# Kernel tuning notes

Measured on AMD Instinct MI355X. Metric: run time of the kernel, lower is better.

Reference implementation:

```python
import jax, jax.numpy as jnp
import numpy as np

IN_DIM = 128
OUT_DIM = 256
N_ETYPES = 4
N_STEPS = 8
B = 128
N_NODES = 256
E = 393216
CONCAT = IN_DIM + OUT_DIM


def _conv1d(x, w, b):
    # x: [B, C, L], w: [O, I, K] -> valid conv, stride 1
    y = jax.lax.conv_general_dilated(x, w, (1,), 'VALID', dimension_numbers=('NCH', 'OIH', 'NCH'))
    return y + b[None, :, None]


def _maxpool1d(x, k, s):
    return jax.lax.reduce_window(x, -jnp.inf, jax.lax.max, (1, 1, k), (1, 1, s), 'VALID')


def setup_inputs():
    key = jax.random.key(0)
    ks = jax.random.split(key, 16)
    Nn = B * N_NODES
    sc = 0.05
    f32 = jnp.float32
    return {
        'features': jax.random.normal(ks[0], (Nn, IN_DIM), f32),
        'src': jax.random.randint(ks[1], (E,), 0, Nn),
        'dst': jax.random.randint(ks[2], (E,), 0, Nn),
        'etype': jax.random.randint(ks[3], (E,), 0, N_ETYPES),
        'W_msg': jax.random.normal(ks[4], (N_ETYPES, OUT_DIM, OUT_DIM), f32) * sc,
        'b_msg': jnp.zeros((N_ETYPES, OUT_DIM), f32),
        'gru_Wi': jax.random.normal(ks[5], (OUT_DIM, 3 * OUT_DIM), f32) * sc,
        'gru_Wh': jax.random.normal(ks[6], (OUT_DIM, 3 * OUT_DIM), f32) * sc,
        'gru_bi': jnp.zeros((3 * OUT_DIM,), f32),
        'gru_bh': jnp.zeros((3 * OUT_DIM,), f32),
        'conv1_w': jax.random.normal(ks[7], (OUT_DIM, OUT_DIM, 3), f32) * sc,
        'conv1_b': jnp.zeros((OUT_DIM,), f32),
        'conv2_w': jax.random.normal(ks[8], (OUT_DIM, OUT_DIM, 1), f32) * sc,
        'conv2_b': jnp.zeros((OUT_DIM,), f32),
        'convc1_w': jax.random.normal(ks[9], (CONCAT, CONCAT, 3), f32) * sc,
        'convc1_b': jnp.zeros((CONCAT,), f32),
        'convc2_w': jax.random.normal(ks[10], (CONCAT, CONCAT, 1), f32) * sc,
        'convc2_b': jnp.zeros((CONCAT,), f32),
        'wy': jax.random.normal(ks[11], (OUT_DIM, 1), f32) * sc,
        'by': jnp.zeros((1,), f32),
        'wz': jax.random.normal(ks[12], (CONCAT, 1), f32) * sc,
        'bz': jnp.zeros((1,), f32),
        'num_graphs': B,
    }


def reference(features, src, dst, etype, W_msg, b_msg, gru_Wi, gru_Wh, gru_bi, gru_bh,
              conv1_w, conv1_b, conv2_w, conv2_b, convc1_w, convc1_b, convc2_w, convc2_b,
              wy, by, wz, bz, num_graphs):
    Nn = features.shape[0]
    # DGL GatedGraphConv: pad input feats up to out_feats
    h = jnp.pad(features, ((0, 0), (0, OUT_DIM - IN_DIM)))
    for _ in range(N_STEPS):
        # per-etype linear transform of all nodes: [Nn, T, O]
        H_all = jnp.einsum('nd,tdo->nto', h, W_msg) + b_msg[None]
        msg = H_all[src, etype]                              # [E, O]
        a = jax.ops.segment_sum(msg, dst, num_segments=Nn)   # [Nn, O]
        gi = a @ gru_Wi + gru_bi
        gh = h @ gru_Wh + gru_bh
        ir, iz, ig = jnp.split(gi, 3, axis=-1)
        hr, hz, hg = jnp.split(gh, 3, axis=-1)
        r = jax.nn.sigmoid(ir + hr)
        z = jax.nn.sigmoid(iz + hz)
        g = jnp.tanh(ig + r * hg)
        h = (1.0 - z) * g + z * h
    x_i = features.reshape(num_graphs, -1, IN_DIM)
    h_i = h.reshape(num_graphs, -1, OUT_DIM)
    c_i = jnp.concatenate([h_i, x_i], axis=-1)
    Y1 = _maxpool1d(jax.nn.relu(_conv1d(h_i.transpose(0, 2, 1), conv1_w, conv1_b)), 3, 2)
    Y2 = _maxpool1d(jax.nn.relu(_conv1d(Y1, conv2_w, conv2_b)), 2, 2).transpose(0, 2, 1)
    Z1 = _maxpool1d(jax.nn.relu(_conv1d(c_i.transpose(0, 2, 1), convc1_w, convc1_b)), 3, 2)
    Z2 = _maxpool1d(jax.nn.relu(_conv1d(Z1, convc2_w, convc2_b)), 2, 2).transpose(0, 2, 1)
    before_avg = (Y2 @ wy + by) * (Z2 @ wz + bz)   # [B, L, 1]
    avg = before_avg.mean(axis=1)                    # [B, 1]
    return jax.nn.sigmoid(avg).squeeze(-1)           # [B]
```

## Files before the change

kernel.cpp:

```cpp
#include <hip/hip_runtime.h>

#define DEV static __device__ __forceinline__

typedef float f32x4 __attribute__((ext_vector_type(4)));
typedef __bf16 bf16x8 __attribute__((ext_vector_type(8)));
typedef unsigned int u32x4 __attribute__((ext_vector_type(4)));
typedef unsigned int u32x2 __attribute__((ext_vector_type(2)));

#define NNODE 32768
#define NEDGE 393216

DEV unsigned short f2bf(float f) {
    unsigned int u = __builtin_bit_cast(unsigned int, f);
    u += 0x7FFFu + ((u >> 16) & 1u);
    return (unsigned short)(u >> 16);
}
DEV float bf2f(unsigned int b) {
    unsigned int u = b << 16;
    return __builtin_bit_cast(float, u);
}
DEV unsigned int pk2(float a, float b) {
    return (unsigned int)f2bf(a) | ((unsigned int)f2bf(b) << 16);
}
DEV float sigf(float x) { return 1.f / (1.f + __expf(-x)); }

DEV void gld16(const void* g, void* l) {
    __builtin_amdgcn_global_load_lds(
        (const __attribute__((address_space(1))) void*)(g),
        (__attribute__((address_space(3))) void*)(l),
        16, 0, 0);
}


__global__ __launch_bounds__(256) void init_k(
    const float* __restrict__ feat,
    unsigned short* __restrict__ hb0, unsigned short* __restrict__ hb1,
    unsigned short* __restrict__ fb)
{
    int idx = blockIdx.x * 256 + threadIdx.x;
    int r = idx >> 8, c = idx & 255;
    float f = 0.f;
    if (r < NNODE && c < 128) f = feat[(size_t)r * 128 + c];
    unsigned short v = f2bf(f);
    hb0[(size_t)r * 256 + c] = v;
    hb1[(size_t)r * 256 + c] = v;
    if (c < 128) fb[(size_t)r * 128 + c] = v;
}

__global__ __launch_bounds__(256) void prep_wmsg_k(
    const float* __restrict__ Wm, unsigned short* __restrict__ WT)
{
    int idx = blockIdx.x * 256 + threadIdx.x;
    int j = idx >> 8, d = idx & 255;
    int t = j >> 8, o = j & 255;
    WT[idx] = f2bf(Wm[t * 65536 + d * 256 + o]);
}

__global__ __launch_bounds__(256) void prep_gru_k(
    const float* __restrict__ Wi, const float* __restrict__ Wh,
    unsigned short* __restrict__ B2T)
{
    int idx = blockIdx.x * 256 + threadIdx.x;
    int j = idx >> 9, k = idx & 511;
    int band = j >> 6, g = (j >> 4) & 3, ch = (band << 4) + (j & 15);
    float v = 0.f;
    if (g == 0) v = (k < 256) ? Wi[k * 768 + ch] : Wh[(k - 256) * 768 + ch];
    else if (g == 1) v = (k < 256) ? Wi[k * 768 + 256 + ch] : Wh[(k - 256) * 768 + 256 + ch];
    else if (g == 2) { if (k < 256) v = Wi[k * 768 + 512 + ch]; }
    else { if (k >= 256) v = Wh[(k - 256) * 768 + 512 + ch]; }
    B2T[idx] = f2bf(v);
}

__global__ __launch_bounds__(256) void prep_bias2_k(
    const float* __restrict__ bi, const float* __restrict__ bh,
    float* __restrict__ b2)
{
    int j = blockIdx.x * 256 + threadIdx.x;
    int band = j >> 6, g = (j >> 4) & 3, ch = (band << 4) + (j & 15);
    float v;
    if (g == 0) v = bi[ch] + bh[ch];
    else if (g == 1) v = bi[256 + ch] + bh[256 + ch];
    else if (g == 2) v = bi[512 + ch];
    else v = bh[512 + ch];
    b2[j] = v;
}

__global__ __launch_bounds__(256) void prep_conv_k(
    const float* __restrict__ c1w, const float* __restrict__ c2w,
    const float* __restrict__ cc1w, const float* __restrict__ cc2w,
    unsigned short* __restrict__ BTY, unsigned short* __restrict__ BT2,
    unsigned short* __restrict__ BTZ, unsigned short* __restrict__ BTc2)
{
    int idx = blockIdx.x * 256 + threadIdx.x;
    if (idx < 196608) {
        int o = idx / 768, kk = idx - o * 768, k = kk >> 8, c = kk & 255;
        BTY[idx] = f2bf(c1w[o * 768 + c * 3 + k]);
    } else if (idx < 262144) {
        int r = idx - 196608, o = r >> 8, c = r & 255;
        BT2[r] = f2bf(c2w[o * 256 + c]);
    } else if (idx < 704512) {
        int jx = idx - 262144, o = jx / 1152, kk = jx - o * 1152;
        float v;
        if (kk < 768) { int k = kk >> 8, c = kk & 255; v = cc1w[o * 1152 + c * 3 + k]; }
        else { int r = kk - 768, kf = r >> 7, cf = r & 127; v = cc1w[o * 1152 + (256 + cf) * 3 + kf]; }
        BTZ[jx] = f2bf(v);
    } else {
        int r = idx - 704512, o = r / 384, c = r - o * 384;
        BTc2[r] = f2bf(cc2w[o * 384 + c]);
    }
}


__global__ __launch_bounds__(256) void count_k(
    const int* __restrict__ dst, int* __restrict__ cnt)
{
    int e = blockIdx.x * 256 + threadIdx.x;
    atomicAdd(&cnt[dst[e]], 1);
}

__global__ __launch_bounds__(1024) void scan1_k(
    const int* __restrict__ cnt, int* __restrict__ rp, int* __restrict__ bsum)
{
    __shared__ int buf[1024];
    int b = blockIdx.x, tid = threadIdx.x;
    int n = (b << 10) + tid;
    int v = cnt[n];
    buf[tid] = v;
    __syncthreads();
    for (int off = 1; off < 1024; off <<= 1) {
        int x = (tid >= off) ? buf[tid - off] : 0;
        __syncthreads();
        buf[tid] += x;
        __syncthreads();
    }
    rp[n] = buf[tid] - v;
    if (tid == 1023) bsum[b] = buf[1023];
}

__global__ __launch_bounds__(64) void scan2_k(
    const int* __restrict__ bsum, int* __restrict__ boff, int* __restrict__ rp)
{
    int lane = threadIdx.x;
    int v = (lane < 32) ? bsum[lane] : 0;
    int s = v;
    #pragma unroll
    for (int off = 1; off < 32; off <<= 1) {
        int x = __shfl_up(s, off, 64);
        if (lane >= off) s += x;
    }
    if (lane < 32) boff[lane] = s - v;
    if (lane == 31) rp[NNODE] = s;
}

__global__ __launch_bounds__(1024) void scan3_k(
    int* __restrict__ rp, const int* __restrict__ boff)
{
    int b = blockIdx.x, tid = threadIdx.x;
    rp[(b << 10) + tid] += boff[b];
}

__global__ __launch_bounds__(256) void fill_k(
    const int* __restrict__ src, const int* __restrict__ dst,
    const int* __restrict__ et, const int* __restrict__ rp,
    int* __restrict__ pos, int* __restrict__ edat)
{
    int e = blockIdx.x * 256 + threadIdx.x;
    int d = dst[e];
    int p = atomicAdd(&pos[d], 1);
    edat[rp[d] + p] = src[e] | (et[e] << 20);
}


__global__ __launch_bounds__(256) void agg2_k(
    const int* __restrict__ rp, const int* __restrict__ edat,
    const unsigned short* __restrict__ Hmsg, unsigned short* __restrict__ Aonly)
{
    int wave = threadIdx.x >> 6, lane = threadIdx.x & 63;
    int n = (blockIdx.x << 2) + wave;
    int e0 = rp[n], e1 = rp[n + 1];
    float a0 = 0.f, a1 = 0.f, a2 = 0.f, a3 = 0.f;
    const unsigned short* hc = Hmsg + (lane << 2);
    int e = e0;
    for (; e + 8 <= e1; e += 8) {
        u32x2 v[8];
        #pragma unroll
        for (int q = 0; q < 8; q++) {
            int d = edat[e + q];
            v[q] = *(const u32x2*)(hc + ((size_t)(d & 0xFFFFF) << 10) + ((d >> 20) << 8));
        }
        #pragma unroll
        for (int q = 0; q < 8; q++) {
            a0 += bf2f(v[q].x & 0xFFFFu); a1 += bf2f(v[q].x >> 16);
            a2 += bf2f(v[q].y & 0xFFFFu); a3 += bf2f(v[q].y >> 16);
        }
    }
    for (; e < e1; e++) {
        int d = edat[e];
        u32x2 v = *(const u32x2*)(hc + ((size_t)(d & 0xFFFFF) << 10) + ((d >> 20) << 8));
        a0 += bf2f(v.x & 0xFFFFu); a1 += bf2f(v.x >> 16);
        a2 += bf2f(v.y & 0xFFFFu); a3 += bf2f(v.y >> 16);
    }
    u32x2 p; p.x = pk2(a0, a1); p.y = pk2(a2, a3);
    *(u32x2*)(Aonly + (size_t)n * 256 + (lane << 2)) = p;
}

#define STAGE_COORDS                                            \
    int srow[4], scb[4], soff[4];                               \
    _Pragma("unroll")                                           \
    for (int p = 0; p < 4; p++) {                               \
        int c = wave + p * 4;                                   \
        int half = c >> 3, cc = c & 7;                          \
        srow[p] = cc * 16 + (lane >> 2);                        \
        scb[p] = (((lane & 3) ^ ((lane >> 3) & 3)) + half * 4) * 8; \
        soff[p] = half * 4096 + cc * 512;                       \
    }

#define MFMA64(AS, BS)                                                        \
    _Pragma("unroll")                                                         \
    for (int h = 0; h < 2; h++) {                                             \
        bf16x8 af[4], bfr[4];                                                 \
        _Pragma("unroll")                                                     \
        for (int i = 0; i < 4; i++)                                           \
            af[i] = *(const bf16x8*)(&AS[h * 4096 + (qm + i * 16 + fm) * 32 + fksw * 8]); \
        _Pragma("unroll")                                                     \
        for (int i = 0; i < 4; i++)                                           \
            bfr[i] = *(const bf16x8*)(&BS[h * 4096 + (qn + i * 16 + fm) * 32 + fksw * 8]); \
        _Pragma("unroll")                                                     \
        for (int i = 0; i < 4; i++)                                           \
            _Pragma("unroll")                                                 \
            for (int j = 0; j < 4; j++)                                       \
                acc[i][j] = __builtin_amdgcn_mfma_f32_16x16x32_bf16(bfr[j], af[i], acc[i][j], 0, 0, 0); \
    }

__global__ __launch_bounds__(256) void gemm_bt(
    const unsigned short* __restrict__ A, int lda,
    const unsigned short* __restrict__ Bt,
    unsigned short* __restrict__ Cb, int ldcb,
    const float* __restrict__ bias,
    int N, int K, int swz, int relu)
{
    __shared__ __align__(16) unsigned short As[128 * 64];
    __shared__ __align__(16) unsigned short Bs[128 * 64];
    const int tid = threadIdx.x;
    int id = blockIdx.x;
    if (swz) { int per = gridDim.x >> 3; id = (id & 7) * per + (id >> 3); }
    const int nb = N >> 7;
    const int bm = id / nb, bn = id - bm * nb;
    const int wave = tid >> 6, lane = tid & 63;
    const unsigned short* Ag = A + (size_t)(bm * 128) * lda;
    const unsigned short* Bg = Bt + (size_t)(bn * 128) * K;
    const int qm = (wave & 1) << 6, qn = (wave >> 1) << 6;
    const int fm = lane & 15, fkv = lane >> 4;
    const int fksw = fkv ^ ((fm >> 1) & 3);
    STAGE_COORDS

    f32x4 acc[4][4] = {};

    for (int kb = 0; kb < K; kb += 64) {
        __syncthreads();
        #pragma unroll
        for (int p = 0; p < 4; p++)
            gld16(Ag + (size_t)srow[p] * lda + kb + scb[p], As + soff[p]);
        #pragma unroll
        for (int p = 0; p < 4; p++)
            gld16(Bg + (size_t)srow[p] * K + kb + scb[p], Bs + soff[p]);
        __syncthreads();
        MFMA64(As, Bs)
    }

    const int m0 = bm * 128 + qm + fm;
    const int n0 = bn * 128 + qn + (fkv << 2);
    #pragma unroll
    for (int i = 0; i < 4; i++) {
        int row = m0 + i * 16;
        #pragma unroll
        for (int j = 0; j < 4; j++) {
            int col = n0 + j * 16;
            float v0 = acc[i][j][0], v1 = acc[i][j][1],
                  v2 = acc[i][j][2], v3 = acc[i][j][3];
            if (bias) {
                float4 bv = *(const float4*)(bias + col);
                v0 += bv.x; v1 += bv.y; v2 += bv.z; v3 += bv.w;
            }
            if (relu) {
                v0 = fmaxf(v0, 0.f); v1 = fmaxf(v1, 0.f);
                v2 = fmaxf(v2, 0.f); v3 = fmaxf(v3, 0.f);
            }
            u32x2 p; p.x = pk2(v0, v1); p.y = pk2(v2, v3);
            *(u32x2*)(Cb + (size_t)row * ldcb + col) = p;
        }
    }
}

__global__ __launch_bounds__(256) void gemm_conv(
    const unsigned short* __restrict__ Ah,
    const unsigned short* __restrict__ Af,
    const unsigned short* __restrict__ Bt,
    unsigned short* __restrict__ Cb, int ldcb,
    const float* __restrict__ bias,
    int N, int K)
{
    __shared__ __align__(16) unsigned short As[128 * 64];
    __shared__ __align__(16) unsigned short Bs[128 * 64];
    const int tid = threadIdx.x;
    int id = blockIdx.x;
    { int per = gridDim.x >> 3; id = (id & 7) * per + (id >> 3); }
    const int nb = N >> 7;
    const int bm = id / nb, bn = id - bm * nb;
    const int wave = tid >> 6, lane = tid & 63;
    const unsigned short* Bg = Bt + (size_t)(bn * 128) * K;
    const int qm = (wave & 1) << 6, qn = (wave >> 1) << 6;
    const int fm = lane & 15, fkv = lane >> 4;
    const int fksw = fkv ^ ((fm >> 1) & 3);
    STAGE_COORDS

    f32x4 acc[4][4] = {};

    for (int kb = 0; kb < K; kb += 64) {
        const unsigned short* base; int ldA, col, shift;
        if (kb < 768) { base = Ah; ldA = 256; shift = kb >> 8; col = kb & 255; }
        else { int r = kb - 768; base = Af; ldA = 128; shift = r >> 7; col = r & 127; }
        const unsigned short* Ag = base + (size_t)(bm * 128 + shift) * ldA + col;
        __syncthreads();
        #pragma unroll
        for (int p = 0; p < 4; p++)
            gld16(Ag + (size_t)srow[p] * ldA + scb[p], As + soff[p]);
        #pragma unroll
        for (int p = 0; p < 4; p++)
            gld16(Bg + (size_t)srow[p] * K + kb + scb[p], Bs + soff[p]);
        __syncthreads();
        MFMA64(As, Bs)
    }

    const int m0 = bm * 128 + qm + fm;
    const int n0 = bn * 128 + qn + (fkv << 2);
    #pragma unroll
    for (int i = 0; i < 4; i++) {
        int row = m0 + i * 16;
        #pragma unroll
        for (int j = 0; j < 4; j++) {
            int col = n0 + j * 16;
            float4 bv = *(const float4*)(bias + col);
            float v0 = fmaxf(acc[i][j][0] + bv.x, 0.f);
            float v1 = fmaxf(acc[i][j][1] + bv.y, 0.f);
            float v2 = fmaxf(acc[i][j][2] + bv.z, 0.f);
            float v3 = fmaxf(acc[i][j][3] + bv.w, 0.f);
            u32x2 p; p.x = pk2(v0, v1); p.y = pk2(v2, v3);
            *(u32x2*)(Cb + (size_t)row * ldcb + col) = p;
        }
    }
}

__global__ __launch_bounds__(256) void gemm_gru(
    const unsigned short* __restrict__ Aonly,
    const unsigned short* __restrict__ hbc,
    const unsigned short* __restrict__ Bt,
    const float* __restrict__ b2p,
    unsigned short* __restrict__ hbn)
{
    __shared__ __align__(16) unsigned short As[128 * 64];
    __shared__ __align__(16) unsigned short Bs[128 * 64];
    const int tid = threadIdx.x;
    int id = blockIdx.x;
    { int per = gridDim.x >> 3; id = (id & 7) * per + (id >> 3); }
    const int bm = id >> 3;
    const int bn = id & 7;
    const int wave = tid >> 6, lane = tid & 63;
    const unsigned short* Bg = Bt + (size_t)(bn * 128) * 512;
    const int qm = (wave & 1) << 6, qn = (wave >> 1) << 6;
    const int fm = lane & 15, fkv = lane >> 4;
    const int fksw = fkv ^ ((fm >> 1) & 3);
    STAGE_COORDS

    f32x4 acc[4][4] = {};

    #pragma unroll
    for (int kb = 0; kb < 512; kb += 64) {
        const unsigned short* base = (kb < 256) ? Aonly : hbc;
        const unsigned short* Ag = base + (size_t)(bm * 128) * 256 + (kb & 255);
        __syncthreads();
        #pragma unroll
        for (int p = 0; p < 4; p++)
            gld16(Ag + (size_t)srow[p] * 256 + scb[p], As + soff[p]);
        #pragma unroll
        for (int p = 0; p < 4; p++)
            gld16(Bg + (size_t)srow[p] * 512 + kb + scb[p], Bs + soff[p]);
        __syncthreads();
        MFMA64(As, Bs)
    }

    const int band = (bn << 1) + (qn >> 6);
    const int chb = (band << 4) + (fkv << 2);
    const float4 brv = *(const float4*)(b2p + (band << 6) + 0  + (fkv << 2));
    const float4 bzv = *(const float4*)(b2p + (band << 6) + 16 + (fkv << 2));
    const float4 bgv = *(const float4*)(b2p + (band << 6) + 32 + (fkv << 2));
    const float4 bhv = *(const float4*)(b2p + (band << 6) + 48 + (fkv << 2));
    const float br_[4] = {brv.x, brv.y, brv.z, brv.w};
    const float bz_[4] = {bzv.x, bzv.y, bzv.z, bzv.w};
    const float bg_[4] = {bgv.x, bgv.y, bgv.z, bgv.w};
    const float bh_[4] = {bhv.x, bhv.y, bhv.z, bhv.w};
    const int m0 = bm * 128 + qm + fm;
    #pragma unroll
    for (int i = 0; i < 4; i++) {
        int row = m0 + i * 16;
        u32x2 hv = *(const u32x2*)(hbc + (size_t)row * 256 + chb);
        float hp[4] = {bf2f(hv.x & 0xFFFFu), bf2f(hv.x >> 16),
                       bf2f(hv.y & 0xFFFFu), bf2f(hv.y >> 16)};
        float hn[4];
        #pragma unroll
        for (int r = 0; r < 4; r++) {
            float rg = sigf(acc[i][0][r] + br_[r]);
            float zz = sigf(acc[i][1][r] + bz_[r]);
            float pre = acc[i][2][r] + bg_[r] + rg * (acc[i][3][r] + bh_[r]);
            pre = fminf(fmaxf(pre, -15.f), 15.f);
            float t = __expf(2.f * pre);
            float gq = (t - 1.f) / (t + 1.f);
            hn[r] = (1.f - zz) * gq + zz * hp[r];
        }
        u32x2 p; p.x = pk2(hn[0], hn[1]); p.y = pk2(hn[2], hn[3]);
        *(u32x2*)(hbn + (size_t)row * 256 + chb) = p;
    }
}

__global__ __launch_bounds__(256) void pool_k(
    const unsigned short* __restrict__ in, int ldin, int Lb_in, int L_out,
    int win, int C,
    unsigned short* __restrict__ ob, int ldo)
{
    int idx = blockIdx.x * 256 + threadIdx.x;
    int c = idx % C;
    int row = idx / C;
    int b = row / L_out, lp = row - b * L_out;
    const unsigned short* p = in + (size_t)(b * Lb_in + 2 * lp) * ldin + c;
    float m = bf2f(p[0]);
    for (int d = 1; d < win; d++) m = fmaxf(m, bf2f(p[(size_t)d * ldin]));
    ob[(size_t)row * ldo + c] = f2bf(m);
}

__global__ __launch_bounds__(64) void final_k(
    const unsigned short* __restrict__ CY, const unsigned short* __restrict__ CZ,
    const float* __restrict__ wy, const float* __restrict__ by,
    const float* __restrict__ wz, const float* __restrict__ bz,
    float* __restrict__ out)
{
    int b = blockIdx.x, lane = threadIdx.x;
    float val = 0.f;
    if (lane < 63) {
        const unsigned short* y0 = CY + (size_t)(b * 126 + 2 * lane) * 256;
        const unsigned short* y1 = y0 + 256;
        float y = 0.f;
        for (int o = 0; o < 256; o++)
            y += fmaxf(bf2f(y0[o]), bf2f(y1[o])) * wy[o];
        y += by[0];
        const unsigned short* z0 = CZ + (size_t)(b * 126 + 2 * lane) * 384;
        const unsigned short* z1 = z0 + 384;
        float z = 0.f;
        for (int o = 0; o < 384; o++)
            z += fmaxf(bf2f(z0[o]), bf2f(z1[o])) * wz[o];
        z += bz[0];
        val = y * z;
    }
    for (int off = 32; off > 0; off >>= 1) val += __shfl_down(val, off, 64);
    if (lane == 0) out[b] = sigf(val * (1.f / 63.f));
}


extern "C" void kernel_launch(void* const* d_in, const int* in_sizes, int n_in,
                              void* d_out, int out_size, void* d_ws, size_t ws_size,
                              hipStream_t stream)
{
    const float* feat = (const float*)d_in[0];
    const int* src = (const int*)d_in[1];
    const int* dst = (const int*)d_in[2];
    const int* et  = (const int*)d_in[3];
    const float* Wm  = (const float*)d_in[4];
    const float* bm  = (const float*)d_in[5];
    const float* Wi  = (const float*)d_in[6];
    const float* Wh  = (const float*)d_in[7];
    const float* bi  = (const float*)d_in[8];
    const float* bh  = (const float*)d_in[9];
    const float* c1w = (const float*)d_in[10];
    const float* c1b = (const float*)d_in[11];
    const float* c2w = (const float*)d_in[12];
    const float* c2b = (const float*)d_in[13];
    const float* cc1w = (const float*)d_in[14];
    const float* cc1b = (const float*)d_in[15];
    const float* cc2w = (const float*)d_in[16];
    const float* cc2b = (const float*)d_in[17];
    const float* wy = (const float*)d_in[18];
    const float* by = (const float*)d_in[19];
    const float* wz = (const float*)d_in[20];
    const float* bz = (const float*)d_in[21];
    float* out = (float*)d_out;

    char* w = (char*)d_ws;
    size_t off = 0;
    auto alloc = [&](size_t bytes) -> char* {
        char* p = w + off; off += (bytes + 255) & ~(size_t)255; return p;
    };
    unsigned short* hb0 = (unsigned short*)alloc((size_t)(NNODE + 8) * 256 * 2);
    unsigned short* hb1 = (unsigned short*)alloc((size_t)(NNODE + 8) * 256 * 2);
    unsigned short* fb  = (unsigned short*)alloc((size_t)(NNODE + 8) * 128 * 2);
    unsigned short* Aonly = (unsigned short*)alloc((size_t)NNODE * 256 * 2);
    char* R = alloc((size_t)NNODE * 1024 * 2);
    unsigned short* Hmsg = (unsigned short*)R;
    unsigned short* CbY  = (unsigned short*)R;
    unsigned short* CbZ  = (unsigned short*)(R + (size_t)NNODE * 256 * 2);
    unsigned short* P    = (unsigned short*)alloc((size_t)16128 * 384 * 2);
    unsigned short* Cb2Y = (unsigned short*)alloc((size_t)16128 * 256 * 2);
    unsigned short* Cb2Z = (unsigned short*)alloc((size_t)16128 * 384 * 2);
    unsigned short* WT   = (unsigned short*)alloc(1024 * 256 * 2);
    unsigned short* B2T  = (unsigned short*)alloc(1024 * 512 * 2);
    float* b2            = (float*)alloc(1024 * 4);
    unsigned short* BTY  = (unsigned short*)alloc(256 * 768 * 2);
    unsigned short* BT2  = (unsigned short*)alloc(256 * 256 * 2);
    unsigned short* BTZ  = (unsigned short*)alloc(384 * 1152 * 2);
    unsigned short* BTc2 = (unsigned short*)alloc(384 * 384 * 2);
    int* rp     = (int*)alloc((NNODE + 1) * 4);
    int* pos    = (int*)alloc(NNODE * 4);
    int* cnt    = (int*)alloc(NNODE * 4);
    int* bsum   = (int*)alloc(32 * 4);
    int* boff   = (int*)alloc(32 * 4);
    int* edat   = (int*)alloc(NEDGE * 4);

    hipLaunchKernelGGL(init_k, dim3(NNODE + 8), dim3(256), 0, stream, feat, hb0, hb1, fb);
    hipLaunchKernelGGL(prep_wmsg_k, dim3(1024), dim3(256), 0, stream, Wm, WT);
    hipLaunchKernelGGL(prep_gru_k, dim3(2048), dim3(256), 0, stream, Wi, Wh, B2T);
    hipLaunchKernelGGL(prep_bias2_k, dim3(4), dim3(256), 0, stream, bi, bh, b2);
    hipLaunchKernelGGL(prep_conv_k, dim3(3328), dim3(256), 0, stream,
                       c1w, c2w, cc1w, cc2w, BTY, BT2, BTZ, BTc2);
    hipMemsetAsync(pos, 0, NNODE * 4, stream);
    hipMemsetAsync(cnt, 0, NNODE * 4, stream);
    hipLaunchKernelGGL(count_k, dim3(NEDGE / 256), dim3(256), 0, stream, dst, cnt);
    hipLaunchKernelGGL(scan1_k, dim3(32), dim3(1024), 0, stream, cnt, rp, bsum);
    hipLaunchKernelGGL(scan2_k, dim3(1), dim3(64), 0, stream, bsum, boff, rp);
    hipLaunchKernelGGL(scan3_k, dim3(32), dim3(1024), 0, stream, rp, boff);
    hipLaunchKernelGGL(fill_k, dim3(NEDGE / 256), dim3(256), 0, stream, src, dst, et, rp, pos, edat);

    unsigned short* hbuf[2] = {hb0, hb1};
    for (int step = 0; step < 8; step++) {
        unsigned short* cur = hbuf[step & 1];
        unsigned short* nxt = hbuf[(step + 1) & 1];
        hipLaunchKernelGGL(gemm_bt, dim3(2048), dim3(256), 0, stream,
            cur, 256, WT, Hmsg, 1024, bm, 1024, 256, 1, 0);
        hipLaunchKernelGGL(agg2_k, dim3(NNODE / 4), dim3(256), 0, stream, rp, edat, Hmsg, Aonly);
        hipLaunchKernelGGL(gemm_gru, dim3(2048), dim3(256), 0, stream,
            Aonly, cur, B2T, b2, nxt);
    }

    hipLaunchKernelGGL(gemm_conv, dim3(512), dim3(256), 0, stream,
        hb0, (const unsigned short*)nullptr, BTY, CbY, 256, c1b, 256, 768);
    hipLaunchKernelGGL(pool_k, dim3(16128), dim3(256), 0, stream,
        CbY, 256, 256, 126, 3, 256, P, 256);
    hipLaunchKernelGGL(gemm_bt, dim3(252), dim3(256), 0, stream,
        P, 256, BT2, Cb2Y, 256, c2b, 256, 256, 0, 1);

    hipLaunchKernelGGL(gemm_conv, dim3(768), dim3(256), 0, stream,
        hb0, fb, BTZ, CbZ, 384, cc1b, 384, 1152);
    hipLaunchKernelGGL(pool_k, dim3(24192), dim3(256), 0, stream,
        CbZ, 384, 256, 126, 3, 384, P, 384);
    hipLaunchKernelGGL(gemm_bt, dim3(378), dim3(256), 0, stream,
        P, 384, BTc2, Cb2Z, 384, cc2b, 384, 384, 0, 1);

    hipLaunchKernelGGL(final_k, dim3(128), dim3(64), 0, stream,
        Cb2Y, Cb2Z, wy, by, wz, bz, out);
}
```

Measured before the change: 1.308 ms.

## Replace per-step GEMMs with 256x256-tile double-buffered pipelined MFMA kernel

Introduces a templated gemm256 kernel with 256x256 output tiles, 8 waves, and double-buffered LDS (128KB). Global loads for the next K-tile are interleaved with MFMA phases using explicit waitcnt, barriers and setprio. It replaces both the message GEMM and the fused GRU GEMM in the 8-step loop, raising data reuse per tile and overlapping loads with compute. Risks include higher register and LDS pressure limiting occupancy, and fewer blocks (512) across the CUs.

Measured after the change: 1.230 ms. 6.0% less time.

```diff
diff --git a/kernel.cpp b/kernel.cpp
--- a/kernel.cpp
+++ b/kernel.cpp
@@ -351,74 +351,171 @@
     }
 }
 
-__global__ __launch_bounds__(256) void gemm_gru(
-    const unsigned short* __restrict__ Aonly,
-    const unsigned short* __restrict__ hbc,
+
+#define VM2 asm volatile("s_waitcnt vmcnt(2)" ::: "memory");
+#define VM0 asm volatile("s_waitcnt vmcnt(0)" ::: "memory");
+
+#define PH(ASP, BSP, MH, NH, LOADA, STG, VM)                                   \
+  {                                                                            \
+    if (LOADA) {                                                               \
+      _Pragma("unroll")                                                        \
+      for (int i_ = 0; i_ < 4; i_++) {                                         \
+        af[i_][0] = *(const bf16x8*)&(ASP)[((wm << 7) + ((MH) << 6) + (i_ << 4) + fm) * 32 + fof];        \
+        af[i_][1] = *(const bf16x8*)&(ASP)[8192 + ((wm << 7) + ((MH) << 6) + (i_ << 4) + fm) * 32 + fof]; \
+      }                                                                        \
+    }                                                                          \
+    _Pragma("unroll")                                                          \
+    for (int j_ = 0; j_ < 2; j_++) {                                           \
+      bfr[j_][0] = *(const bf16x8*)&(BSP)[((wn << 6) + ((NH) << 5) + (j_ << 4) + fm) * 32 + fof];        \
+      bfr[j_][1] = *(const bf16x8*)&(BSP)[8192 + ((wn << 6) + ((NH) << 5) + (j_ << 4) + fm) * 32 + fof]; \
+    }                                                                          \
+    STG                                                                        \
+    __builtin_amdgcn_sched_barrier(0);                                         \
+    VM                                                                         \
+    __builtin_amdgcn_s_barrier();                                              \
+    asm volatile("s_waitcnt lgkmcnt(0)" ::: "memory");                         \
+    __builtin_amdgcn_sched_barrier(0);                                         \
+    __builtin_amdgcn_s_setprio(1);                                             \
+    _Pragma("unroll")                                                          \
+    for (int i_ = 0; i_ < 4; i_++)                                             \
+      _Pragma("unroll")                                                        \
+      for (int j_ = 0; j_ < 2; j_++) {                                         \
+        acc[((MH) << 2) + i_][((NH) << 1) + j_] =                              \
+          __builtin_amdgcn_mfma_f32_16x16x32_bf16(bfr[j_][0], af[i_][0],       \
+            acc[((MH) << 2) + i_][((NH) << 1) + j_], 0, 0, 0);                 \
+        acc[((MH) << 2) + i_][((NH) << 1) + j_] =                              \
+          __builtin_amdgcn_mfma_f32_16x16x32_bf16(bfr[j_][1], af[i_][1],       \
+            acc[((MH) << 2) + i_][((NH) << 1) + j_], 0, 0, 0);                 \
+      }                                                                        \
+    __builtin_amdgcn_s_setprio(0);                                             \
+    __builtin_amdgcn_s_barrier();                                              \
+    __builtin_amdgcn_sched_barrier(0);                                         \
+  }
+
+template<int K, int EPI>
+__global__ __launch_bounds__(512, 2) void gemm256(
+    const unsigned short* __restrict__ Aa,
+    const unsigned short* __restrict__ Ab,
     const unsigned short* __restrict__ Bt,
-    const float* __restrict__ b2p,
-    unsigned short* __restrict__ hbn)
-{
-    __shared__ __align__(16) unsigned short As[128 * 64];
-    __shared__ __align__(16) unsigned short Bs[128 * 64];
+    const float* __restrict__ bias,
+    unsigned short* __restrict__ Cb, int ldcb, int N)
+{
+    constexpr int NT = K / 64;
+    __shared__ __align__(16) unsigned short LDS[65536];
+    unsigned short* AsE = LDS;
+    unsigned short* BsE = LDS + 16384;
+    unsigned short* AsO = LDS + 32768;
+    unsigned short* BsO = LDS + 49152;
+
     const int tid = threadIdx.x;
     int id = blockIdx.x;
     { int per = gridDim.x >> 3; id = (id & 7) * per + (id >> 3); }
-    const int bm = id >> 3;
-    const int bn = id & 7;
-    const int wave = tid >> 6, lane = tid & 63;
-    const unsigned short* Bg = Bt + (size_t)(bn * 128) * 512;
-    const int qm = (wave & 1) << 6, qn = (wave >> 1) << 6;
+    const int nb = N >> 8;
+    const int bm = id / nb, bn = id - bm * nb;
+    const int wv = tid >> 6, lane = tid & 63;
+    const int wm = wv >> 2, wn = wv & 3;
     const int fm = lane & 15, fkv = lane >> 4;
-    const int fksw = fkv ^ ((fm >> 1) & 3);
-    STAGE_COORDS
-
-    f32x4 acc[4][4] = {};
+    const int fof = ((fkv ^ ((fm >> 1) & 3)) << 3);
+    const int cOff = (((lane & 3) ^ ((lane >> 3) & 3)) << 3);
+    const int lq = lane >> 2;
+
+    const unsigned short* AgA = Aa + ((size_t)(bm << 8)) * 256;
+    const unsigned short* AgB = (EPI == 1) ? (Ab + ((size_t)(bm << 8)) * 256)
+                                           : (const unsigned short*)nullptr;
+    const unsigned short* Bg = Bt + ((size_t)(bn << 8)) * K;
+
+    auto stA = [&](int kt, int h) {
+        const unsigned short* g = (kt < 4) ? AgA : AgB;
+        const int kcol = (kt & 3) << 6;
+        unsigned short* lt = (kt & 1) ? AsO : AsE;
+        const int sr = ((wv & 3) << 4) + ((wv >> 2) << 7) + (h << 6);
+        const unsigned short* gp = g + (size_t)(sr + lq) * 256 + kcol + cOff;
+        unsigned short* lp = lt + (sr << 5);
+        gld16(gp, lp);
+        gld16(gp + 32, lp + 8192);
+    };
+    auto stB = [&](int kt, int h) {
+        unsigned short* lt = (kt & 1) ? BsO : BsE;
+        const int sr = ((wv & 1) << 4) + ((wv >> 1) << 6) + (h << 5);
+        const unsigned short* gp = Bg + (size_t)(sr + lq) * K + (kt << 6) + cOff;
+        unsigned short* lp = lt + (sr << 5);
+        gld16(gp, lp);
+        gld16(gp + 32, lp + 8192);
+    };
+
+    f32x4 acc[8][4] = {};
+    bf16x8 af[4][2], bfr[2][2];
+
+    stA(0, 0); stB(0, 0); stA(0, 1); stB(0, 1); stA(1, 0);
+    asm volatile("s_waitcnt vmcnt(2)" ::: "memory");
+    __builtin_amdgcn_s_barrier();
+    __builtin_amdgcn_sched_barrier(0);
 
     #pragma unroll
-    for (int kb = 0; kb < 512; kb += 64) {
-        const unsigned short* base = (kb < 256) ? Aonly : hbc;
-        const unsigned short* Ag = base + (size_t)(bm * 128) * 256 + (kb & 255);
-        __syncthreads();
-        #pragma unroll
-        for (int p = 0; p < 4; p++)
-            gld16(Ag + (size_t)srow[p] * 256 + scb[p], As + soff[p]);
-        #pragma unroll
-        for (int p = 0; p < 4; p++)
-            gld16(Bg + (size_t)srow[p] * 512 + kb + scb[p], Bs + soff[p]);
-        __syncthreads();
-        MFMA64(As, Bs)
-    }
-
-    const int band = (bn << 1) + (qn >> 6);
-    const int chb = (band << 4) + (fkv << 2);
-    const float4 brv = *(const float4*)(b2p + (band << 6) + 0  + (fkv << 2));
-    const float4 bzv = *(const float4*)(b2p + (band << 6) + 16 + (fkv << 2));
-    const float4 bgv = *(const float4*)(b2p + (band << 6) + 32 + (fkv << 2));
-    const float4 bhv = *(const float4*)(b2p + (band << 6) + 48 + (fkv << 2));
-    const float br_[4] = {brv.x, brv.y, brv.z, brv.w};
-    const float bz_[4] = {bzv.x, bzv.y, bzv.z, bzv.w};
-    const float bg_[4] = {bgv.x, bgv.y, bgv.z, bgv.w};
-    const float bh_[4] = {bhv.x, bhv.y, bhv.z, bhv.w};
-    const int m0 = bm * 128 + qm + fm;
-    #pragma unroll
-    for (int i = 0; i < 4; i++) {
-        int row = m0 + i * 16;
-        u32x2 hv = *(const u32x2*)(hbc + (size_t)row * 256 + chb);
-        float hp[4] = {bf2f(hv.x & 0xFFFFu), bf2f(hv.x >> 16),
-                       bf2f(hv.y & 0xFFFFu), bf2f(hv.y >> 16)};
-        float hn[4];
-        #pragma unroll
-        for (int r = 0; r < 4; r++) {
-            float rg = sigf(acc[i][0][r] + br_[r]);
-            float zz = sigf(acc[i][1][r] + bz_[r]);
-            float pre = acc[i][2][r] + bg_[r] + rg * (acc[i][3][r] + bh_[r]);
-            pre = fminf(fmaxf(pre, -15.f), 15.f);
-            float t = __expf(2.f * pre);
-            float gq = (t - 1.f) / (t + 1.f);
-            hn[r] = (1.f - zz) * gq + zz * hp[r];
+    for (int t = 0; t < NT / 2; t++) {
+        const int kt1 = 2 * t + 1, kt2 = 2 * t + 2, kt3 = 2 * t + 3;
+        PH(AsE, BsE, 0, 0, 1, { stB(kt1, 0); }, ;)
+        PH(AsE, BsE, 0, 1, 0, { stA(kt1, 1); }, ;)
+        PH(AsE, BsE, 1, 0, 1, { stB(kt1, 1); }, ;)
+        if (kt2 < NT) { PH(AsE, BsE, 1, 1, 0, { stA(kt2, 0); }, VM2) }
+        else          { PH(AsE, BsE, 1, 1, 0, ;, VM0) }
+        PH(AsO, BsO, 0, 0, 1, { if (kt2 < NT) stB(kt2, 0); }, ;)
+        PH(AsO, BsO, 0, 1, 0, { if (kt2 < NT) stA(kt2, 1); }, ;)
+        PH(AsO, BsO, 1, 0, 1, { if (kt2 < NT) stB(kt2, 1); }, ;)
+        if (kt3 < NT) { PH(AsO, BsO, 1, 1, 0, { stA(kt3, 0); }, VM2) }
+        else          { PH(AsO, BsO, 1, 1, 0, ;, VM0) }
+    }
+
+    if constexpr (EPI == 0) {
+        const int m0 = (bm << 8) + (wm << 7) + fm;
+        const int n0 = (bn << 8) + (wn << 6) + (fkv << 2);
+        #pragma unroll
+        for (int i = 0; i < 8; i++) {
+            const int row = m0 + (i << 4);
+            #pragma unroll
+            for (int j = 0; j < 4; j++) {
+                const int col = n0 + (j << 4);
+                const float4 bv = *(const float4*)(bias + col);
+                float v0 = acc[i][j][0] + bv.x;
+                float v1 = acc[i][j][1] + bv.y;
+                float v2 = acc[i][j][2] + bv.z;
+                float v3 = acc[i][j][3] + bv.w;
+                u32x2 p; p.x = pk2(v0, v1); p.y = pk2(v2, v3);
+                *(u32x2*)(Cb + (size_t)row * ldcb + col) = p;
+            }
         }
-        u32x2 p; p.x = pk2(hn[0], hn[1]); p.y = pk2(hn[2], hn[3]);
-        *(u32x2*)(hbn + (size_t)row * 256 + chb) = p;
+    } else {
+        const int band = (bn << 2) + wn;
+        const int chb = (band << 4) + (fkv << 2);
+        const float4 brv = *(const float4*)(bias + (band << 6) + 0  + (fkv << 2));
+        const float4 bzv = *(const float4*)(bias + (band << 6) + 16 + (fkv << 2));
+        const float4 bgv = *(const float4*)(bias + (band << 6) + 32 + (fkv << 2));
+        const float4 bhv = *(const float4*)(bias + (band << 6) + 48 + (fkv << 2));
+        const float br_[4] = {brv.x, brv.y, brv.z, brv.w};
+        const float bz_[4] = {bzv.x, bzv.y, bzv.z, bzv.w};
+        const float bg_[4] = {bgv.x, bgv.y, bgv.z, bgv.w};
+        const float bh_[4] = {bhv.x, bhv.y, bhv.z, bhv.w};
+        const int m0 = (bm << 8) + (wm << 7) + fm;
+        #pragma unroll
+        for (int i = 0; i < 8; i++) {
+            const int row = m0 + (i << 4);
+            u32x2 hv = *(const u32x2*)(Ab + (size_t)row * 256 + chb);
+            float hp[4] = {bf2f(hv.x & 0xFFFFu), bf2f(hv.x >> 16),
+                           bf2f(hv.y & 0xFFFFu), bf2f(hv.y >> 16)};
+            float hn[4];
+            #pragma unroll
+            for (int r = 0; r < 4; r++) {
+                float rg = sigf(acc[i][0][r] + br_[r]);
+                float zz = sigf(acc[i][1][r] + bz_[r]);
+                float pre = acc[i][2][r] + bg_[r] + rg * (acc[i][3][r] + bh_[r]);
+                pre = fminf(fmaxf(pre, -15.f), 15.f);
+                float tt = __expf(2.f * pre);
+                float gq = (tt - 1.f) / (tt + 1.f);
+                hn[r] = (1.f - zz) * gq + zz * hp[r];
+            }
+            u32x2 p; p.x = pk2(hn[0], hn[1]); p.y = pk2(hn[2], hn[3]);
+            *(u32x2*)(Cb + (size_t)row * 256 + chb) = p;
+        }
     }
 }
 
@@ -541,11 +638,11 @@
     for (int step = 0; step < 8; step++) {
         unsigned short* cur = hbuf[step & 1];
         unsigned short* nxt = hbuf[(step + 1) & 1];
-        hipLaunchKernelGGL(gemm_bt, dim3(2048), dim3(256), 0, stream,
-            cur, 256, WT, Hmsg, 1024, bm, 1024, 256, 1, 0);
+        hipLaunchKernelGGL((gemm256<256, 0>), dim3(512), dim3(512), 0, stream,
+            cur, (const unsigned short*)nullptr, WT, bm, Hmsg, 1024, 1024);
         hipLaunchKernelGGL(agg2_k, dim3(NNODE / 4), dim3(256), 0, stream, rp, edat, Hmsg, Aonly);
-        hipLaunchKernelGGL(gemm_gru, dim3(2048), dim3(256), 0, stream,
-            Aonly, cur, B2T, b2, nxt);
+        hipLaunchKernelGGL((gemm256<512, 1>), dim3(512), dim3(512), 0, stream,
+            Aonly, cur, B2T, b2, nxt, 256, 1024);
     }
 
     hipLaunchKernelGGL(gemm_conv, dim3(512), dim3(256), 0, stream,
```

## Double-buffer LDS tiles in the three bf16 MFMA GEMM kernels

Applied to the files above, without the earlier changes.

Converts the gemm_bt, gemm_conv and gemm_gru main loops from single-buffered shared-memory staging to ping-pong buffers. The next K-slice is issued into the spare buffer before the MFMAs on the current one, and each iteration needs only one barrier instead of two. The aim is to hide global-load latency behind matrix math and cut barrier stalls. The cost is twice the LDS per block, which may lower occupancy, plus extra pointer-swap logic.

Result: no change. 1.323 ms (+1.1%).

```diff
diff --git a/kernel.cpp b/kernel.cpp
--- a/kernel.cpp
+++ b/kernel.cpp
@@ -221,10 +221,10 @@
         bf16x8 af[4], bfr[4];                                                 \
         _Pragma("unroll")                                                     \
         for (int i = 0; i < 4; i++)                                           \
-            af[i] = *(const bf16x8*)(&AS[h * 4096 + (qm + i * 16 + fm) * 32 + fksw * 8]); \
+            af[i] = *(const bf16x8*)(&(AS)[h * 4096 + (qm + i * 16 + fm) * 32 + fksw * 8]); \
         _Pragma("unroll")                                                     \
         for (int i = 0; i < 4; i++)                                           \
-            bfr[i] = *(const bf16x8*)(&BS[h * 4096 + (qn + i * 16 + fm) * 32 + fksw * 8]); \
+            bfr[i] = *(const bf16x8*)(&(BS)[h * 4096 + (qn + i * 16 + fm) * 32 + fksw * 8]); \
         _Pragma("unroll")                                                     \
         for (int i = 0; i < 4; i++)                                           \
             _Pragma("unroll")                                                 \
@@ -239,8 +239,10 @@
     const float* __restrict__ bias,
     int N, int K, int swz, int relu)
 {
-    __shared__ __align__(16) unsigned short As[128 * 64];
-    __shared__ __align__(16) unsigned short Bs[128 * 64];
+    __shared__ __align__(16) unsigned short As0[128 * 64];
+    __shared__ __align__(16) unsigned short As1[128 * 64];
+    __shared__ __align__(16) unsigned short Bs0[128 * 64];
+    __shared__ __align__(16) unsigned short Bs1[128 * 64];
     const int tid = threadIdx.x;
     int id = blockIdx.x;
     if (swz) { int per = gridDim.x >> 3; id = (id & 7) * per + (id >> 3); }
@@ -254,18 +256,28 @@
     const int fksw = fkv ^ ((fm >> 1) & 3);
     STAGE_COORDS
 
+    auto stageA = [&](int kb, unsigned short* dst) {
+        #pragma unroll
+        for (int p = 0; p < 4; p++)
+            gld16(Ag + (size_t)srow[p] * lda + kb + scb[p], dst + soff[p]);
+    };
+    auto stageB = [&](int kb, unsigned short* dst) {
+        #pragma unroll
+        for (int p = 0; p < 4; p++)
+            gld16(Bg + (size_t)srow[p] * K + kb + scb[p], dst + soff[p]);
+    };
+
     f32x4 acc[4][4] = {};
 
+    stageA(0, As0); stageB(0, Bs0);
+    __syncthreads();
+    unsigned short *Ac = As0, *An = As1, *Bc = Bs0, *Bn = Bs1;
     for (int kb = 0; kb < K; kb += 64) {
+        if (kb + 64 < K) { stageA(kb + 64, An); stageB(kb + 64, Bn); }
+        MFMA64(Ac, Bc)
         __syncthreads();
-        #pragma unroll
-        for (int p = 0; p < 4; p++)
-            gld16(Ag + (size_t)srow[p] * lda + kb + scb[p], As + soff[p]);
-        #pragma unroll
-        for (int p = 0; p < 4; p++)
-            gld16(Bg + (size_t)srow[p] * K + kb + scb[p], Bs + soff[p]);
-        __syncthreads();
-        MFMA64(As, Bs)
+        { auto t = Ac; Ac = An; An = t; }
+        { auto t = Bc; Bc = Bn; Bn = t; }
     }
 
     const int m0 = bm * 128 + qm + fm;
@@ -300,8 +312,10 @@
     const float* __restrict__ bias,
     int N, int K)
 {
-    __shared__ __align__(16) unsigned short As[128 * 64];
-    __shared__ __align__(16) unsigned short Bs[128 * 64];
+    __shared__ __align__(16) unsigned short As0[128 * 64];
+    __shared__ __align__(16) unsigned short As1[128 * 64];
+    __shared__ __align__(16) unsigned short Bs0[128 * 64];
+    __shared__ __align__(16) unsigned short Bs1[128 * 64];
     const int tid = threadIdx.x;
     int id = blockIdx.x;
     { int per = gridDim.x >> 3; id = (id & 7) * per + (id >> 3); }
@@ -314,22 +328,32 @@
     const int fksw = fkv ^ ((fm >> 1) & 3);
     STAGE_COORDS
 
-    f32x4 acc[4][4] = {};
-
-    for (int kb = 0; kb < K; kb += 64) {
+    auto stageA = [&](int kb, unsigned short* dst) {
         const unsigned short* base; int ldA, col, shift;
         if (kb < 768) { base = Ah; ldA = 256; shift = kb >> 8; col = kb & 255; }
         else { int r = kb - 768; base = Af; ldA = 128; shift = r >> 7; col = r & 127; }
         const unsigned short* Ag = base + (size_t)(bm * 128 + shift) * ldA + col;
+        #pragma unroll
+        for (int p = 0; p < 4; p++)
+            gld16(Ag + (size_t)srow[p] * ldA + scb[p], dst + soff[p]);
+    };
+    auto stageB = [&](int kb, unsigned short* dst) {
+        #pragma unroll
+        for (int p = 0; p < 4; p++)
+            gld16(Bg + (size_t)srow[p] * K + kb + scb[p], dst + soff[p]);
+    };
+
+    f32x4 acc[4][4] = {};
+
+    stageA(0, As0); stageB(0, Bs0);
+    __syncthreads();
+    unsigned short *Ac = As0, *An = As1, *Bc = Bs0, *Bn = Bs1;
+    for (int kb = 0; kb < K; kb += 64) {
+        if (kb + 64 < K) { stageA(kb + 64, An); stageB(kb + 64, Bn); }
+        MFMA64(Ac, Bc)
         __syncthreads();
-        #pragma unroll
-        for (int p = 0; p < 4; p++)
-            gld16(Ag + (size_t)srow[p] * ldA + scb[p], As + soff[p]);
-        #pragma unroll
-        for (int p = 0; p < 4; p++)
-            gld16(Bg + (size_t)srow[p] * K + kb + scb[p], Bs + soff[p]);
-        __syncthreads();
-        MFMA64(As, Bs)
+        { auto t = Ac; Ac = An; An = t; }
+        { auto t = Bc; Bc = Bn; Bn = t; }
     }
 
     const int m0 = bm * 128 + qm + fm;
@@ -358,8 +382,10 @@
     const float* __restrict__ b2p,
     unsigned short* __restrict__ hbn)
 {
-    __shared__ __align__(16) unsigned short As[128 * 64];
-    __shared__ __align__(16) unsigned short Bs[128 * 64];
+    __shared__ __align__(16) unsigned short As0[128 * 64];
+    __shared__ __align__(16) unsigned short As1[128 * 64];
+    __shared__ __align__(16) unsigned short Bs0[128 * 64];
+    __shared__ __align__(16) unsigned short Bs1[128 * 64];
     const int tid = threadIdx.x;
     int id = blockIdx.x;
     { int per = gridDim.x >> 3; id = (id & 7) * per + (id >> 3); }
@@ -372,21 +398,31 @@
     const int fksw = fkv ^ ((fm >> 1) & 3);
     STAGE_COORDS
 
+    auto stageA = [&](int kb, unsigned short* dst) {
+        const unsigned short* base = (kb < 256) ? Aonly : hbc;
+        const unsigned short* Ag = base + (size_t)(bm * 128) * 256 + (kb & 255);
+        #pragma unroll
+        for (int p = 0; p < 4; p++)
+            gld16(Ag + (size_t)srow[p] * 256 + scb[p], dst + soff[p]);
+    };
+    auto stageB = [&](int kb, unsigned short* dst) {
+        #pragma unroll
+        for (int p = 0; p < 4; p++)
+            gld16(Bg + (size_t)srow[p] * 512 + kb + scb[p], dst + soff[p]);
+    };
+
     f32x4 acc[4][4] = {};
 
+    stageA(0, As0); stageB(0, Bs0);
+    __syncthreads();
+    unsigned short *Ac = As0, *An = As1, *Bc = Bs0, *Bn = Bs1;
     #pragma unroll
     for (int kb = 0; kb < 512; kb += 64) {
-        const unsigned short* base = (kb < 256) ? Aonly : hbc;
-        const unsigned short* Ag = base + (size_t)(bm * 128) * 256 + (kb & 255);
+        if (kb < 448) { stageA(kb + 64, An); stageB(kb + 64, Bn); }
+        MFMA64(Ac, Bc)
         __syncthreads();
-        #pragma unroll
-        for (int p = 0; p < 4; p++)
-            gld16(Ag + (size_t)srow[p] * 256 + scb[p], As + soff[p]);
-        #pragma unroll
-        for (int p = 0; p < 4; p++)
-            gld16(Bg + (size_t)srow[p] * 512 + kb + scb[p], Bs + soff[p]);
-        __syncthreads();
-        MFMA64(As, Bs)
+        { auto t = Ac; Ac = An; An = t; }
+        { auto t = Bc; Bc = Bn; Bn = t; }
     }
 
     const int band = (bn << 1) + (qn >> 6);
```
